# Performance work log

Measured on AMD Instinct MI355X. Metric: run time of the kernel, lower is better.

The kernel has to match this reference:

```python
import jax, jax.numpy as jnp
import numpy as np

B, N, F_NODE = 16, 48, 5
H1, H2 = 32, 64
D_ATT = H2 * 3  # 192


def setup_inputs() -> dict:
    rng = np.random.default_rng(0)
    n_nodes = B * N
    # complete graph per batch element; each directed pair appears with class 0 and class 1,
    # ordered by (src, dst, class) so that filtering src>dst leaves a sorted list where
    # consecutive rows are the (class0, class1) pair of the same undirected edge.
    i, j = np.meshgrid(np.arange(N), np.arange(N), indexing="ij")
    m = i != j
    pi = np.repeat(i[m], 2)
    pj = np.repeat(j[m], 2)
    cls = np.tile(np.array([0.0, 1.0], np.float32), N * (N - 1))
    offs = np.arange(B)[:, None] * N
    src = (pi[None] + offs).ravel()
    dst = (pj[None] + offs).ravel()
    edges = jnp.asarray(np.stack([src, dst]).astype(np.int64))
    w = rng.random(src.shape[0]).astype(np.float32)
    edge_attr = jnp.asarray(np.stack([w, np.tile(cls, B)], axis=1))
    x = jnp.asarray(rng.standard_normal((n_nodes, F_NODE)).astype(np.float32))
    detector_labels = jnp.ones((n_nodes,), bool)
    batch_labels = jnp.asarray(np.repeat(np.arange(B), N).astype(np.int64))

    def lin(k_out, k_in):
        s = 1.0 / np.sqrt(k_in)
        return (jnp.asarray(rng.uniform(-s, s, (k_out, k_in)).astype(np.float32)),
                jnp.asarray(rng.uniform(-s, s, (k_out,)).astype(np.float32)))

    W_we, b_we = lin(1, 3)
    Wrel1, brel1 = lin(H1, F_NODE); Wroot1, _ = lin(H1, F_NODE)
    Wrel2, brel2 = lin(H2, H1);     Wroot2, _ = lin(H2, H1)
    W_ee, b_ee = lin(H2, 3)
    W_qkv, b_qkv = lin(3 * D_ATT, D_ATT)
    W_in, b_in = lin(3 * D_ATT, D_ATT)
    W_out, b_out = lin(D_ATT, D_ATT)
    W_o, b_o = lin(1, D_ATT)
    return dict(x=x, edges=edges, edge_attr=edge_attr,
                detector_labels=detector_labels, batch_labels=batch_labels,
                W_we=W_we, b_we=b_we, Wrel1=Wrel1, brel1=brel1, Wroot1=Wroot1,
                Wrel2=Wrel2, brel2=brel2, Wroot2=Wroot2,
                W_ee=W_ee, b_ee=b_ee, W_qkv=W_qkv, b_qkv=b_qkv,
                W_in=W_in, b_in=b_in, W_out=W_out, b_out=b_out,
                W_o=W_o, b_o=b_o)


def _graph_conv(x, src, dst, w, Wrel, brel, Wroot, n_nodes):
    # pyg GraphConv: lin_rel(sum_{j->i} e_ji * x_j) + lin_root(x_i)
    msg = x[src] * w  # w: [E,1] scalar edge weight
    agg = jax.ops.segment_sum(msg, dst, num_segments=n_nodes)
    return agg @ Wrel.T + brel + x @ Wroot.T


def reference(x, edges, edge_attr, detector_labels, batch_labels,
              W_we, b_we, Wrel1, brel1, Wroot1, Wrel2, brel2, Wroot2,
              W_ee, b_ee, W_qkv, b_qkv, W_in, b_in, W_out, b_out, W_o, b_o):
    n_nodes = x.shape[0]
    E = edges.shape[1]
    src, dst = edges[0], edges[1]
    # edge weight embedding from (weight, one_hot(class))
    c = jax.nn.one_hot(edge_attr[:, 1].astype(jnp.int32), 2, dtype=x.dtype)
    w = jax.nn.relu(jnp.concatenate([edge_attr[:, :1], c], -1) @ W_we.T + b_we)  # [E,1]
    x = jax.nn.relu(_graph_conv(x, src, dst, w, Wrel1, brel1, Wroot1, n_nodes))
    x = jax.nn.relu(_graph_conv(x, src, dst, w, Wrel2, brel2, Wroot2, n_nodes))
    # keep one direction (src > dst): construction guarantees exactly E//2 kept, already sorted
    keep = jnp.nonzero(src > dst, size=E // 2)[0]
    srcK, dstK, ea = src[keep], dst[keep], edge_attr[keep]
    c = jax.nn.one_hot(ea[:, 1].astype(jnp.int32), 2, dtype=x.dtype)
    wK = jax.nn.relu(jnp.concatenate([ea[:, :1], c], -1) @ W_ee.T + b_ee)  # [Ek,H2]
    feat = jnp.concatenate([x[srcK], wK, x[dstK]], -1)  # [Ek, 3*H2]
    # equal-size graphs -> unbatch + pad_sequence == reshape (no padding)
    S = feat.shape[0] // B
    feat = feat.reshape(B, S, -1)
    e_src = srcK.reshape(B, S)
    e_dst = dstK.reshape(B, S)
    classes = ea[:, 1].reshape(B, S, 1)
    pad_mask = e_src == e_dst  # all False (no ragged padding here)
    # SelfAttention: extra qkv projection, then 1-head MultiheadAttention
    qkv = feat @ W_qkv.T + b_qkv
    q, k, v = jnp.split(qkv, 3, -1)
    Wq, Wk, Wv = jnp.split(W_in, 3, 0)
    bq, bk, bv = jnp.split(b_in, 3, 0)
    q = q @ Wq.T + bq; k = k @ Wk.T + bk; v = v @ Wv.T + bv
    scores = jnp.einsum("bqd,bkd->bqk", q, k) / jnp.sqrt(jnp.asarray(q.shape[-1], q.dtype))
    scores = jnp.where(pad_mask[:, None, :], -jnp.inf, scores)
    attn = jax.nn.softmax(scores, -1)
    feat = jnp.einsum("bqk,bkd->bqd", attn, v) @ W_out.T + b_out
    # SplitSyndromes with all-True detector_labels keeps every edge (identity)
    logit = feat @ W_o.T + b_o  # [B,S,1]
    pair = jnp.concatenate([logit[:, ::2], logit[:, 1::2]], -1)   # [B,S/2,2]
    cls2 = jnp.concatenate([classes[:, ::2], classes[:, 1::2]], -1)
    min_inds = jnp.argmin(pair, axis=2, keepdims=True)
    ef = jnp.take_along_axis(pair, min_inds, 2)   # min values, [B,S/2,1]
    ec = jnp.take_along_axis(cls2, min_inds, 2)
    e4s = jnp.stack([e_src[:, ::2], e_src[:, 1::2]], -1)  # [B,S/2,2]
    e4t = jnp.stack([e_dst[:, ::2], e_dst[:, 1::2]], -1)
    out_src = jnp.take_along_axis(e4s, min_inds, -1)
    out_dst = jnp.take_along_axis(e4t, min_inds, -1)
    out_edges = jnp.concatenate([out_src, out_dst], -1)
    return out_edges, ef, ec
```

## Files before the change

### kernel.cpp

```cpp
#include <hip/hip_runtime.h>
#include <hip/hip_bf16.h>

typedef __hip_bfloat16 bf16;
typedef __attribute__((ext_vector_type(8))) short short8;
typedef __attribute__((ext_vector_type(16))) float float16v;
typedef __attribute__((ext_vector_type(2))) float float2v;

#define B_     16
#define N_     48
#define NODES  768
#define PAIRS  2256
#define EK     36096
#define S_     2256
#define SH     1128
#define D_     192
#define KITERS 71
#define QTILES 71
#define QSCALE 0.10411754f

__device__ __forceinline__ float bf(const bf16* p, int i) { return __bfloat162float(p[i]); }
__device__ __forceinline__ float u2f(unsigned short u) {
    return __uint_as_float(((unsigned int)u) << 16);
}
__device__ __forceinline__ float sanitize(float v) {
    if (v > -1e4f && v < 1e4f) return v;
    if (v >= 1e4f) return 1e4f;
    if (v <= -1e4f) return -1e4f;
    return 0.f;
}

__global__ __launch_bounds__(256) void stage1_kernel(
    const bf16* edge_attr, const bf16* W_we, const bf16* b_we, const bf16* x,
    const bf16* Wrel1, const bf16* brel1, const bf16* Wroot1,
    const bf16* Wrel2, const bf16* brel2, const bf16* Wroot2,
    const bf16* W_o, const bf16* b_o, const bf16* W_out, const bf16* b_out,
    const bf16* W_in, const bf16* b_in, const bf16* b_qkv, const bf16* W_qkv,
    float* x2out, float* wo_eff, float* bq_eff, float* bk_eff, float* bv_eff, float* sc,
    float* WqT, float* WkT, bf16* W2b) {
    int blk = blockIdx.x, tid = threadIdx.x;
    if (blk < 16) {
        int b = blk;
        __shared__ float s_ws[N_ * N_];
        __shared__ float s_x[N_ * 5], s_agg1[N_ * 5];
        __shared__ float s_x1[N_ * 32], s_agg2[N_ * 32];
        float we0 = bf(W_we, 0), we1 = bf(W_we, 1), we2 = bf(W_we, 2), bw = bf(b_we, 0);
        for (int idx = tid; idx < N_ * N_; idx += 256) {
            int i = idx / N_, j = idx % N_;
            float v = 0.f;
            if (i != j) {
                int p = i * 47 + (j < i ? j : j - 1);
                int e = (b * PAIRS + p) * 2;
                float w0 = fmaxf(we0 * bf(edge_attr, (e + 0) * 2) + we1 + bw, 0.f);
                float w1 = fmaxf(we0 * bf(edge_attr, (e + 1) * 2) + we2 + bw, 0.f);
                v = w0 + w1;
            }
            s_ws[idx] = v;
        }
        for (int idx = tid; idx < N_ * 5; idx += 256) s_x[idx] = bf(x, b * N_ * 5 + idx);
        __syncthreads();
        if (tid < 240) {
            int j = tid / 5, f = tid % 5;
            float a = 0.f;
            for (int i = 0; i < N_; i++) a += s_ws[i * N_ + j] * s_x[i * 5 + f];
            s_agg1[tid] = a;
        }
        __syncthreads();
        for (int o = tid; o < N_ * 32; o += 256) {
            int j = o >> 5, h = o & 31;
            float a = bf(brel1, h);
            for (int f = 0; f < 5; f++)
                a += bf(Wrel1, h * 5 + f) * s_agg1[j * 5 + f] +
                     bf(Wroot1, h * 5 + f) * s_x[j * 5 + f];
            s_x1[o] = fmaxf(a, 0.f);
        }
        __syncthreads();
        for (int o = tid; o < N_ * 32; o += 256) {
            int j = o >> 5, h = o & 31;
            float a = 0.f;
            for (int i = 0; i < N_; i++) a += s_ws[i * N_ + j] * s_x1[i * 32 + h];
            s_agg2[o] = a;
        }
        __syncthreads();
        for (int o = tid; o < N_ * 64; o += 256) {
            int j = o >> 6, h2 = o & 63;
            float a = bf(brel2, h2);
            for (int h1 = 0; h1 < 32; h1++)
                a += bf(Wrel2, h2 * 32 + h1) * s_agg2[j * 32 + h1] +
                     bf(Wroot2, h2 * 32 + h1) * s_x1[j * 32 + h1];
            x2out[(b * N_ + j) * 64 + h2] = fmaxf(a, 0.f);
        }
    } else if (blk < 209) {
        int a = blk - 16;
        int wave = tid >> 6, lane = tid & 63;
        float partial = 0.f;
        if (a < 192) {
            if (wave == 0) {
                for (int m = lane; m < 192; m += 64)
                    partial += bf(W_o, m) * bf(W_out, m * 192 + a);
            } else {
                int row = (wave - 1) * 192 + a;
                for (int m = lane; m < 192; m += 64)
                    partial += bf(W_in, row * 192 + m) * bf(b_qkv, (wave - 1) * 192 + m);
            }
        } else if (wave == 0) {
            for (int m = lane; m < 192; m += 64) partial += bf(W_o, m) * bf(b_out, m);
        }
        for (int off = 32; off; off >>= 1) partial += __shfl_xor(partial, off, 64);
        if (lane == 0) {
            if (a < 192) {
                if (wave == 0) wo_eff[a] = partial;
                else if (wave == 1) bq_eff[a] = partial + bf(b_in, a);
                else if (wave == 2) bk_eff[a] = partial + bf(b_in, 192 + a);
                else bv_eff[a] = partial + bf(b_in, 384 + a);
            } else if (wave == 0) sc[1] = partial + bf(b_o, 0);
        }
    } else {
        int idx = (blk - 209) * 256 + tid;
        if (idx < D_ * D_) {
            int a = idx / D_, c = idx % D_;
            float acc = 0.f;
            for (int m = 0; m < D_; m++) acc += bf(W_in, a * D_ + m) * bf(W_qkv, m * D_ + c);
            WqT[c * D_ + a] = acc;
            if (c >= 64 && c < 128) W2b[a * 64 + (c - 64)] = __float2bfloat16(acc);
        } else {
            int t = idx - D_ * D_, a = t / D_, c = t % D_;
            float acc = 0.f;
            for (int m = 0; m < D_; m++)
                acc += bf(W_in, (D_ + a) * D_ + m) * bf(W_qkv, (D_ + m) * D_ + c);
            WkT[c * D_ + a] = acc;
            if (c >= 64 && c < 128) W2b[(192 + a) * 64 + (c - 64)] = __float2bfloat16(acc);
        }
    }
}

__global__ __launch_bounds__(256) void stage2_kernel(
    const bf16* W_in, const float* wo_eff, const float* bv_eff,
    const float* x2, const float* WqT, const float* WkT,
    const float* bq_eff, const float* bk_eff,
    float* t_m, float* sc, float* Tq1, float* Tq3, float* Tk1, float* Tk3) {
    int blk = blockIdx.x, tid = threadIdx.x;
    if (blk < 49) {
        int w = blk * 4 + (tid >> 6);
        int lane = tid & 63;
        float partial = 0.f;
        if (w < 192) {
            for (int aa = lane; aa < 192; aa += 64)
                partial += wo_eff[aa] * bf(W_in, (384 + aa) * 192 + w);
        } else if (w == 192) {
            for (int aa = lane; aa < 192; aa += 64) partial += wo_eff[aa] * bv_eff[aa];
        }
        for (int off = 32; off; off >>= 1) partial += __shfl_xor(partial, off, 64);
        if (lane == 0) {
            if (w < 192) t_m[w] = partial;
            else if (w == 192) sc[0] = partial;
        }
    } else {
        int n = blk - 49;
        __shared__ float sx[64];
        if (tid < 64) sx[tid] = x2[n * 64 + tid];
        __syncthreads();
        if (tid < D_) {
            int a = tid;
            float q1 = bq_eff[a], q3 = 0.f, k1 = bk_eff[a], k3 = 0.f;
            for (int c = 0; c < 64; c++) {
                float xv = sx[c];
                q1 += WqT[c * D_ + a] * xv;
                q3 += WqT[(128 + c) * D_ + a] * xv;
                k1 += WkT[c * D_ + a] * xv;
                k3 += WkT[(128 + c) * D_ + a] * xv;
            }
            Tq1[n * D_ + a] = q1; Tq3[n * D_ + a] = q3;
            Tk1[n * D_ + a] = k1; Tk3[n * D_ + a] = k3;
        }
    }
}

__global__ __launch_bounds__(256) void qkvmid_kernel(
    const bf16* edge_attr, const bf16* W_ee, const bf16* b_ee, const bf16* W2b,
    const bf16* W_qkv, const float* t_m, const float* sc, const float* x2,
    const float* Tq1, const float* Tq3, const float* Tk1, const float* Tk3,
    bf16* Q, bf16* K, float* vl) {
    __shared__ short s_w2[384 * 72];
    __shared__ short s_wk[32 * 72];
    __shared__ float s_tm[192], s_wvl[192];
    __shared__ int s_ni[32], s_nj[32];
    __shared__ float s_wraw[32], s_cls[32];
    int tid = threadIdx.x, base = blockIdx.x * 32;

    for (int c = tid; c < 3072; c += 256) {
        int row = c >> 3, off = c & 7;
        uint4 v = *(const uint4*)((const short*)W2b + row * 64 + off * 8);
        *(uint4*)&s_w2[row * 72 + off * 8] = v;
    }
    if (tid < 192) s_tm[tid] = t_m[tid];
    if (tid < 32) {
        int kk_g = base + tid;
        int b = kk_g / S_, kk = kk_g % S_;
        int q = kk >> 1, cls = kk & 1;
        int i = (int)((1.0f + sqrtf(8.0f * (float)q + 1.0f)) * 0.5f);
        while (i * (i - 1) / 2 > q) --i;
        while ((i + 1) * i / 2 <= q) ++i;
        int j = q - i * (i - 1) / 2;
        s_ni[tid] = b * N_ + i; s_nj[tid] = b * N_ + j;
        int e = (b * PAIRS + i * 47 + j) * 2 + cls;
        s_wraw[tid] = bf(edge_attr, e * 2);
        s_cls[tid] = (float)cls;
    }
    __syncthreads();
    for (int idx = tid; idx < 32 * 64; idx += 256) {
        int t = idx >> 6, h = idx & 63;
        int cls = (int)s_cls[t];
        float v = bf(W_ee, h * 3) * s_wraw[t] + bf(W_ee, h * 3 + 1 + cls) + bf(b_ee, h);
        bf16 bv = __float2bfloat16(fmaxf(v, 0.f));
        s_wk[t * 72 + h] = *reinterpret_cast<short*>(&bv);
    }
    if (tid < 192) {
        float acc = 0.f;
        for (int m = 0; m < 192; m++) acc += s_tm[m] * bf(W_qkv, (384 + m) * 192 + tid);
        s_wvl[tid] = acc;
    }
    __syncthreads();

    int wave = tid >> 6, lane = tid & 63;
    int l5 = lane & 31, h5 = lane >> 5;

    short8 af[4];
    #pragma unroll
    for (int kc = 0; kc < 4; kc++)
        af[kc] = *(const short8*)&s_wk[l5 * 72 + kc * 16 + h5 * 8];

    int tl[16], niv[16], njv[16];
    #pragma unroll
    for (int r = 0; r < 16; r++) {
        int t = (r & 3) + 8 * (r >> 2) + 4 * h5;
        tl[r] = t; niv[r] = s_ni[t]; njv[r] = s_nj[t];
    }

    #pragma unroll
    for (int tt = 0; tt < 3; tt++) {
        int ta = wave + tt * 4;
        bool isq = ta < 6;
        int ag = (isq ? ta : ta - 6) * 32 + l5;
        float16v c;
        #pragma unroll
        for (int r = 0; r < 16; r++) c[r] = 0.f;
        #pragma unroll
        for (int kc = 0; kc < 4; kc++) {
            short8 bfr = *(const short8*)&s_w2[(ta * 32 + l5) * 72 + kc * 16 + h5 * 8];
            c = __builtin_amdgcn_mfma_f32_32x32x16_bf16(af[kc], bfr, c, 0, 0, 0);
        }
        const float* T1 = isq ? Tq1 : Tk1;
        const float* T3 = isq ? Tq3 : Tk3;
        bf16* Out = isq ? Q : K;
        #pragma unroll
        for (int r = 0; r < 16; r++) {
            float v = c[r] + T1[niv[r] * D_ + ag] + T3[njv[r] * D_ + ag];
            if (isq) v *= QSCALE;
            Out[(long)(base + tl[r]) * D_ + ag] = __float2bfloat16(v);
        }
    }
    if (tid < 32) {
        float v = sc[0];
        const float* xi = &x2[s_ni[tid] * 64];
        const float* xj = &x2[s_nj[tid] * 64];
        for (int h = 0; h < 64; h++) {
            v += s_wvl[h] * xi[h] + s_wvl[128 + h] * xj[h] +
                 s_wvl[64 + h] * u2f((unsigned short)s_wk[tid * 72 + h]);
        }
        vl[base + tid] = v;
    }
}

__global__ __launch_bounds__(512) void attn_kernel(const bf16* Q, const bf16* K,
                                                   const float* vl, float* part) {
    int x = blockIdx.x;
    int rr = x & 7, rest = x >> 3;
    int hi = rest >= 72;
    int b = rr + 8 * hi;
    int s = rest - 72 * hi;
    int chunk = s / 9, qg = s % 9;
    int tid = threadIdx.x;
    int wave = tid >> 6, lane = tid & 63;
    int n5 = lane & 31, h5 = lane >> 5;
    int qt = qg * 8 + wave;
    bool qvalid = qt < QTILES;
    int t0 = chunk * 9;
    int nit = (chunk == 7) ? 8 : 9;

    __shared__ short s_k[2][32 * 200];
    __shared__ float s_vl[2][32];

    int row0 = tid / 24, cc0 = tid % 24;
    int c1 = tid + 512;
    int row1 = c1 / 24, cc1 = c1 % 24;
    bool has1 = tid < 256;

    short8 qf[12];
    {
        int qrow = b * S_ + qt * 32 + n5;
        if (qrow > B_ * S_ - 1) qrow = B_ * S_ - 1;
        const short* qp = (const short*)Q + (long)qrow * D_;
        #pragma unroll
        for (int kc = 0; kc < 12; kc++) qf[kc] = *(const short8*)(qp + kc * 16 + h5 * 8);
    }

    float lr[16], ar[16];
    #pragma unroll
    for (int r = 0; r < 16; r++) { lr[r] = 0.f; ar[r] = 0.f; }

    uint4 p0, p1; float pv = 0.f;
    {
        int key = t0 * 32 + row0;
        int gk = b * S_ + (key < S_ ? key : S_ - 1);
        p0 = *(const uint4*)((const short*)K + (long)gk * D_ + cc0 * 8);
        if (has1) {
            int key1 = t0 * 32 + row1;
            int gk1 = b * S_ + (key1 < S_ ? key1 : S_ - 1);
            p1 = *(const uint4*)((const short*)K + (long)gk1 * D_ + cc1 * 8);
        }
        if (tid < 32) {
            int key2 = t0 * 32 + tid;
            pv = (key2 < S_) ? vl[b * S_ + key2] : 0.f;
        }
    }

    for (int k = 0; k < nit; ++k) {
        int it = t0 + k;
        int buf = k & 1;
        *(uint4*)&s_k[buf][row0 * 200 + cc0 * 8] = p0;
        if (has1) *(uint4*)&s_k[buf][row1 * 200 + cc1 * 8] = p1;
        if (tid < 32) s_vl[buf][tid] = pv;
        if (k + 1 < nit) {
            int it1 = it + 1;
            int key = it1 * 32 + row0;
            int gk = b * S_ + (key < S_ ? key : S_ - 1);
            p0 = *(const uint4*)((const short*)K + (long)gk * D_ + cc0 * 8);
            if (has1) {
                int key1 = it1 * 32 + row1;
                int gk1 = b * S_ + (key1 < S_ ? key1 : S_ - 1);
                p1 = *(const uint4*)((const short*)K + (long)gk1 * D_ + cc1 * 8);
            }
            if (tid < 32) {
                int key2 = it1 * 32 + tid;
                pv = (key2 < S_) ? vl[b * S_ + key2] : 0.f;
            }
        }
        __syncthreads();
        const short* kb = s_k[buf];
        float16v c;
        #pragma unroll
        for (int r = 0; r < 16; r++) c[r] = 0.f;
        #pragma unroll
        for (int kc = 0; kc < 12; kc++) {
            short8 bfr = *(const short8*)(kb + n5 * 200 + kc * 16 + h5 * 8);
            c = __builtin_amdgcn_mfma_f32_32x32x16_bf16(qf[kc], bfr, c, 0, 0, 0);
        }
        float vlv = s_vl[buf][n5];
        if (it != KITERS - 1) {
            #pragma unroll
            for (int r = 0; r < 16; r++) {
                float p = __builtin_amdgcn_exp2f(c[r]);
                lr[r] += p;
                ar[r] += p * vlv;
            }
        } else {
            bool kv = n5 < 16;
            #pragma unroll
            for (int r = 0; r < 16; r++) {
                float p = kv ? __builtin_amdgcn_exp2f(c[r]) : 0.f;
                lr[r] += p;
                ar[r] += p * vlv;
            }
        }
    }

    if (qvalid) {
        #pragma unroll
        for (int r = 0; r < 16; r++) {
            float l = lr[r], a = ar[r];
            #pragma unroll
            for (int off = 1; off < 32; off <<= 1) {
                l += __shfl_xor(l, off, 64);
                a += __shfl_xor(a, off, 64);
            }
            if (n5 == 0) {
                int qrow = qt * 32 + (r & 3) + 8 * (r >> 2) + 4 * h5;
                if (qrow < S_) {
                    float2v pv2 = {l, a};
                    *(float2v*)&part[((long)(b * S_ + qrow) * 8 + chunk) * 2] = pv2;
                }
            }
        }
    }
}

__global__ __launch_bounds__(256) void final_kernel(const float* part, const float* sc,
                                                    float* out) {
    int idx = blockIdx.x * 256 + threadIdx.x;
    if (idx >= B_ * SH) return;
    int b = idx / SH, p = idx % SH;
    int i = (int)((1.0f + sqrtf(8.0f * (float)p + 1.0f)) * 0.5f);
    while (i * (i - 1) / 2 > p) --i;
    while ((i + 1) * i / 2 <= p) ++i;
    int j = p - i * (i - 1) / 2;
    float co = sc[1];
    float lg[2];
    #pragma unroll
    for (int t = 0; t < 2; t++) {
        long g = (long)b * S_ + 2 * p + t;
        float l = 0.f, a = 0.f;
        #pragma unroll
        for (int c = 0; c < 8; c++) {
            float2v pc = *(const float2v*)&part[(g * 8 + c) * 2];
            l += pc.x;
            a += pc.y;
        }
        lg[t] = sanitize(a / l + co);
    }
    int ind = (lg[1] < lg[0]) ? 1 : 0;
    float ef = ind ? lg[1] : lg[0];
    out[(b * SH + p) * 2 + 0] = (float)(b * N_ + i);
    out[(b * SH + p) * 2 + 1] = (float)(b * N_ + j);
    out[2 * B_ * SH + idx] = ef;
    out[2 * B_ * SH + B_ * SH + idx] = (float)ind;
}

extern "C" void kernel_launch(void* const* d_in, const int* in_sizes, int n_in,
                              void* d_out, int out_size, void* d_ws, size_t ws_size,
                              hipStream_t stream) {
    const bf16* x         = (const bf16*)d_in[0];
    const bf16* edge_attr = (const bf16*)d_in[2];
    const bf16* W_we   = (const bf16*)d_in[5];
    const bf16* b_we   = (const bf16*)d_in[6];
    const bf16* Wrel1  = (const bf16*)d_in[7];
    const bf16* brel1  = (const bf16*)d_in[8];
    const bf16* Wroot1 = (const bf16*)d_in[9];
    const bf16* Wrel2  = (const bf16*)d_in[10];
    const bf16* brel2  = (const bf16*)d_in[11];
    const bf16* Wroot2 = (const bf16*)d_in[12];
    const bf16* W_ee   = (const bf16*)d_in[13];
    const bf16* b_ee   = (const bf16*)d_in[14];
    const bf16* W_qkv  = (const bf16*)d_in[15];
    const bf16* b_qkv  = (const bf16*)d_in[16];
    const bf16* W_in   = (const bf16*)d_in[17];
    const bf16* b_in   = (const bf16*)d_in[18];
    const bf16* W_out  = (const bf16*)d_in[19];
    const bf16* b_out  = (const bf16*)d_in[20];
    const bf16* W_o    = (const bf16*)d_in[21];
    const bf16* b_o    = (const bf16*)d_in[22];

    float* w = (float*)d_ws;
    float* WqT    = w;
    float* WkT    = WqT + 36864;
    float* t_m    = WkT + 36864;
    float* bq_eff = t_m + 192;
    float* bk_eff = bq_eff + 192;
    float* bv_eff = bk_eff + 192;
    float* wo_eff = bv_eff + 192;
    float* sc     = wo_eff + 192;
    float* x2     = sc + 64;
    float* vl     = x2 + 49152;
    float* part   = vl + 36096;
    bf16*  Q      = (bf16*)(part + 577536);
    bf16*  K      = Q + (long)EK * D_;
    bf16*  W2b    = K + (long)EK * D_;
    float* Tq1    = (float*)(W2b + 384 * 64);
    float* Tq3    = Tq1 + NODES * D_;
    float* Tk1    = Tq3 + NODES * D_;
    float* Tk3    = Tk1 + NODES * D_;

    stage1_kernel<<<497, 256, 0, stream>>>(edge_attr, W_we, b_we, x, Wrel1, brel1, Wroot1,
                                           Wrel2, brel2, Wroot2, W_o, b_o, W_out, b_out,
                                           W_in, b_in, b_qkv, W_qkv,
                                           x2, wo_eff, bq_eff, bk_eff, bv_eff, sc,
                                           WqT, WkT, W2b);
    stage2_kernel<<<817, 256, 0, stream>>>(W_in, wo_eff, bv_eff, x2, WqT, WkT,
                                           bq_eff, bk_eff, t_m, sc, Tq1, Tq3, Tk1, Tk3);
    qkvmid_kernel<<<EK / 32, 256, 0, stream>>>(edge_attr, W_ee, b_ee, W2b, W_qkv, t_m, sc, x2,
                                               Tq1, Tq3, Tk1, Tk3, Q, K, vl);
    attn_kernel<<<1152, 512, 0, stream>>>(Q, K, vl, part);
    final_kernel<<<(B_ * SH + 255) / 256, 256, 0, stream>>>(part, sc, (float*)d_out);
}
```

Before: 256.8 us.

## Compute two query tiles per wave in attention and hoist wvl projection

The attention kernel now uses 256-thread blocks where each wave computes two 32-row query tiles against the same K fragment from shared memory, so each K read from LDS feeds twice as many MFMAs. K staging is redistributed over three loads per thread. Separately, the per-block 192x192 wvl reduction that every qkvmid block recomputed is moved into a small dedicated kernel. The vl dot products are also spread over all 256 threads with shuffle reductions. The cost is higher register pressure from doubled Q fragments and accumulators, plus one extra kernel launch.

```diff
diff --git a/kernel.cpp b/kernel.cpp
--- a/kernel.cpp
+++ b/kernel.cpp
@@ -175,14 +175,26 @@
     }
 }
 
+__global__ __launch_bounds__(256) void wvl_kernel(const bf16* W_qkv, const float* t_m,
+                                                  float* wvl) {
+    int w = blockIdx.x * 4 + (threadIdx.x >> 6);
+    int lane = threadIdx.x & 63;
+    if (w >= 192) return;
+    float partial = 0.f;
+    for (int m = lane; m < 192; m += 64)
+        partial += t_m[m] * bf(W_qkv, (384 + m) * 192 + w);
+    for (int off = 32; off; off >>= 1) partial += __shfl_xor(partial, off, 64);
+    if (lane == 0) wvl[w] = partial;
+}
+
 __global__ __launch_bounds__(256) void qkvmid_kernel(
     const bf16* edge_attr, const bf16* W_ee, const bf16* b_ee, const bf16* W2b,
-    const bf16* W_qkv, const float* t_m, const float* sc, const float* x2,
+    const float* wvl, const float* sc, const float* x2,
     const float* Tq1, const float* Tq3, const float* Tk1, const float* Tk3,
     bf16* Q, bf16* K, float* vl) {
     __shared__ short s_w2[384 * 72];
     __shared__ short s_wk[32 * 72];
-    __shared__ float s_tm[192], s_wvl[192];
+    __shared__ float s_wvl[192];
     __shared__ int s_ni[32], s_nj[32];
     __shared__ float s_wraw[32], s_cls[32];
     int tid = threadIdx.x, base = blockIdx.x * 32;
@@ -192,7 +204,7 @@
         uint4 v = *(const uint4*)((const short*)W2b + row * 64 + off * 8);
         *(uint4*)&s_w2[row * 72 + off * 8] = v;
     }
-    if (tid < 192) s_tm[tid] = t_m[tid];
+    if (tid < 192) s_wvl[tid] = wvl[tid];
     if (tid < 32) {
         int kk_g = base + tid;
         int b = kk_g / S_, kk = kk_g % S_;
@@ -214,11 +226,6 @@
         bf16 bv = __float2bfloat16(fmaxf(v, 0.f));
         s_wk[t * 72 + h] = *reinterpret_cast<short*>(&bv);
     }
-    if (tid < 192) {
-        float acc = 0.f;
-        for (int m = 0; m < 192; m++) acc += s_tm[m] * bf(W_qkv, (384 + m) * 192 + tid);
-        s_wvl[tid] = acc;
-    }
     __syncthreads();
 
     int wave = tid >> 6, lane = tid & 63;
@@ -259,20 +266,26 @@
             Out[(long)(base + tl[r]) * D_ + ag] = __float2bfloat16(v);
         }
     }
-    if (tid < 32) {
-        float v = sc[0];
-        const float* xi = &x2[s_ni[tid] * 64];
-        const float* xj = &x2[s_nj[tid] * 64];
-        for (int h = 0; h < 64; h++) {
+    {
+        int t = tid >> 3, g = tid & 7;
+        const float* xi = &x2[s_ni[t] * 64];
+        const float* xj = &x2[s_nj[t] * 64];
+        float v = 0.f;
+        #pragma unroll
+        for (int hh = 0; hh < 8; hh++) {
+            int h = g * 8 + hh;
             v += s_wvl[h] * xi[h] + s_wvl[128 + h] * xj[h] +
-                 s_wvl[64 + h] * u2f((unsigned short)s_wk[tid * 72 + h]);
-        }
-        vl[base + tid] = v;
-    }
-}
-
-__global__ __launch_bounds__(512) void attn_kernel(const bf16* Q, const bf16* K,
-                                                   const float* vl, float* part) {
+                 s_wvl[64 + h] * u2f((unsigned short)s_wk[t * 72 + h]);
+        }
+        v += __shfl_xor(v, 1, 64);
+        v += __shfl_xor(v, 2, 64);
+        v += __shfl_xor(v, 4, 64);
+        if (g == 0) vl[base + t] = v + sc[0];
+    }
+}
+
+__global__ __launch_bounds__(256, 2) void attn_kernel(const bf16* Q, const bf16* K,
+                                                      const float* vl, float* part) {
     int x = blockIdx.x;
     int rr = x & 7, rest = x >> 3;
     int hi = rest >= 72;
@@ -282,109 +295,124 @@
     int tid = threadIdx.x;
     int wave = tid >> 6, lane = tid & 63;
     int n5 = lane & 31, h5 = lane >> 5;
-    int qt = qg * 8 + wave;
-    bool qvalid = qt < QTILES;
+    int qtA = qg * 8 + wave * 2;
+    int qtB = qtA + 1;
+    bool validB = qtB < QTILES;
     int t0 = chunk * 9;
     int nit = (chunk == 7) ? 8 : 9;
 
     __shared__ short s_k[2][32 * 200];
     __shared__ float s_vl[2][32];
 
-    int row0 = tid / 24, cc0 = tid % 24;
-    int c1 = tid + 512;
-    int row1 = c1 / 24, cc1 = c1 % 24;
-    bool has1 = tid < 256;
-
-    short8 qf[12];
+    int r0 = tid / 24, c0 = tid % 24;
+    int r1 = (tid + 256) / 24, c1 = (tid + 256) % 24;
+    int r2 = (tid + 512) / 24, c2 = (tid + 512) % 24;
+
+    short8 qfA[12], qfB[12];
     {
-        int qrow = b * S_ + qt * 32 + n5;
-        if (qrow > B_ * S_ - 1) qrow = B_ * S_ - 1;
-        const short* qp = (const short*)Q + (long)qrow * D_;
-        #pragma unroll
-        for (int kc = 0; kc < 12; kc++) qf[kc] = *(const short8*)(qp + kc * 16 + h5 * 8);
-    }
-
-    float lr[16], ar[16];
+        int qrowA = b * S_ + qtA * 32 + n5;
+        int qrowB = b * S_ + qtB * 32 + n5;
+        if (qrowB > B_ * S_ - 1) qrowB = B_ * S_ - 1;
+        const short* qpA = (const short*)Q + (long)qrowA * D_;
+        const short* qpB = (const short*)Q + (long)qrowB * D_;
+        #pragma unroll
+        for (int kc = 0; kc < 12; kc++) {
+            qfA[kc] = *(const short8*)(qpA + kc * 16 + h5 * 8);
+            qfB[kc] = *(const short8*)(qpB + kc * 16 + h5 * 8);
+        }
+    }
+
+    float lrA[16], arA[16], lrB[16], arB[16];
     #pragma unroll
-    for (int r = 0; r < 16; r++) { lr[r] = 0.f; ar[r] = 0.f; }
-
-    uint4 p0, p1; float pv = 0.f;
+    for (int r = 0; r < 16; r++) { lrA[r] = 0.f; arA[r] = 0.f; lrB[r] = 0.f; arB[r] = 0.f; }
+
+    uint4 p0, p1, p2; float pv = 0.f;
     {
-        int key = t0 * 32 + row0;
-        int gk = b * S_ + (key < S_ ? key : S_ - 1);
-        p0 = *(const uint4*)((const short*)K + (long)gk * D_ + cc0 * 8);
-        if (has1) {
-            int key1 = t0 * 32 + row1;
-            int gk1 = b * S_ + (key1 < S_ ? key1 : S_ - 1);
-            p1 = *(const uint4*)((const short*)K + (long)gk1 * D_ + cc1 * 8);
-        }
+        int k0 = t0 * 32 + r0, k1 = t0 * 32 + r1, k2 = t0 * 32 + r2;
+        p0 = *(const uint4*)((const short*)K + (long)(b * S_ + (k0 < S_ ? k0 : S_ - 1)) * D_ + c0 * 8);
+        p1 = *(const uint4*)((const short*)K + (long)(b * S_ + (k1 < S_ ? k1 : S_ - 1)) * D_ + c1 * 8);
+        p2 = *(const uint4*)((const short*)K + (long)(b * S_ + (k2 < S_ ? k2 : S_ - 1)) * D_ + c2 * 8);
         if (tid < 32) {
-            int key2 = t0 * 32 + tid;
-            pv = (key2 < S_) ? vl[b * S_ + key2] : 0.f;
+            int key = t0 * 32 + tid;
+            pv = (key < S_) ? vl[b * S_ + key] : 0.f;
         }
     }
 
     for (int k = 0; k < nit; ++k) {
         int it = t0 + k;
         int buf = k & 1;
-        *(uint4*)&s_k[buf][row0 * 200 + cc0 * 8] = p0;
-        if (has1) *(uint4*)&s_k[buf][row1 * 200 + cc1 * 8] = p1;
+        *(uint4*)&s_k[buf][r0 * 200 + c0 * 8] = p0;
+        *(uint4*)&s_k[buf][r1 * 200 + c1 * 8] = p1;
+        *(uint4*)&s_k[buf][r2 * 200 + c2 * 8] = p2;
         if (tid < 32) s_vl[buf][tid] = pv;
         if (k + 1 < nit) {
             int it1 = it + 1;
-            int key = it1 * 32 + row0;
-            int gk = b * S_ + (key < S_ ? key : S_ - 1);
-            p0 = *(const uint4*)((const short*)K + (long)gk * D_ + cc0 * 8);
-            if (has1) {
-                int key1 = it1 * 32 + row1;
-                int gk1 = b * S_ + (key1 < S_ ? key1 : S_ - 1);
-                p1 = *(const uint4*)((const short*)K + (long)gk1 * D_ + cc1 * 8);
-            }
+            int k0 = it1 * 32 + r0, k1 = it1 * 32 + r1, k2 = it1 * 32 + r2;
+            p0 = *(const uint4*)((const short*)K + (long)(b * S_ + (k0 < S_ ? k0 : S_ - 1)) * D_ + c0 * 8);
+            p1 = *(const uint4*)((const short*)K + (long)(b * S_ + (k1 < S_ ? k1 : S_ - 1)) * D_ + c1 * 8);
+            p2 = *(const uint4*)((const short*)K + (long)(b * S_ + (k2 < S_ ? k2 : S_ - 1)) * D_ + c2 * 8);
             if (tid < 32) {
-                int key2 = it1 * 32 + tid;
-                pv = (key2 < S_) ? vl[b * S_ + key2] : 0.f;
+                int key = it1 * 32 + tid;
+                pv = (key < S_) ? vl[b * S_ + key] : 0.f;
             }
         }
         __syncthreads();
         const short* kb = s_k[buf];
-        float16v c;
-        #pragma unroll
-        for (int r = 0; r < 16; r++) c[r] = 0.f;
+        float16v cA, cB;
+        #pragma unroll
+        for (int r = 0; r < 16; r++) { cA[r] = 0.f; cB[r] = 0.f; }
         #pragma unroll
         for (int kc = 0; kc < 12; kc++) {
             short8 bfr = *(const short8*)(kb + n5 * 200 + kc * 16 + h5 * 8);
-            c = __builtin_amdgcn_mfma_f32_32x32x16_bf16(qf[kc], bfr, c, 0, 0, 0);
+            cA = __builtin_amdgcn_mfma_f32_32x32x16_bf16(qfA[kc], bfr, cA, 0, 0, 0);
+            cB = __builtin_amdgcn_mfma_f32_32x32x16_bf16(qfB[kc], bfr, cB, 0, 0, 0);
         }
         float vlv = s_vl[buf][n5];
         if (it != KITERS - 1) {
             #pragma unroll
             for (int r = 0; r < 16; r++) {
-                float p = __builtin_amdgcn_exp2f(c[r]);
-                lr[r] += p;
-                ar[r] += p * vlv;
+                float pA = __builtin_amdgcn_exp2f(cA[r]);
+                float pB = __builtin_amdgcn_exp2f(cB[r]);
+                lrA[r] += pA; arA[r] += pA * vlv;
+                lrB[r] += pB; arB[r] += pB * vlv;
             }
         } else {
             bool kv = n5 < 16;
             #pragma unroll
             for (int r = 0; r < 16; r++) {
-                float p = kv ? __builtin_amdgcn_exp2f(c[r]) : 0.f;
-                lr[r] += p;
-                ar[r] += p * vlv;
-            }
-        }
-    }
-
-    if (qvalid) {
+                float pA = kv ? __builtin_amdgcn_exp2f(cA[r]) : 0.f;
+                float pB = kv ? __builtin_amdgcn_exp2f(cB[r]) : 0.f;
+                lrA[r] += pA; arA[r] += pA * vlv;
+                lrB[r] += pB; arB[r] += pB * vlv;
+            }
+        }
+    }
+
+    #pragma unroll
+    for (int r = 0; r < 16; r++) {
+        float l = lrA[r], a = arA[r];
+        #pragma unroll
+        for (int off = 1; off < 32; off <<= 1) {
+            l += __shfl_xor(l, off, 64);
+            a += __shfl_xor(a, off, 64);
+        }
+        if (n5 == 0) {
+            int qrow = qtA * 32 + (r & 3) + 8 * (r >> 2) + 4 * h5;
+            float2v pv2 = {l, a};
+            *(float2v*)&part[((long)(b * S_ + qrow) * 8 + chunk) * 2] = pv2;
+        }
+    }
+    if (validB) {
         #pragma unroll
         for (int r = 0; r < 16; r++) {
-            float l = lr[r], a = ar[r];
+            float l = lrB[r], a = arB[r];
             #pragma unroll
             for (int off = 1; off < 32; off <<= 1) {
                 l += __shfl_xor(l, off, 64);
                 a += __shfl_xor(a, off, 64);
             }
             if (n5 == 0) {
-                int qrow = qt * 32 + (r & 3) + 8 * (r >> 2) + 4 * h5;
+                int qrow = qtB * 32 + (r & 3) + 8 * (r >> 2) + 4 * h5;
                 if (qrow < S_) {
                     float2v pv2 = {l, a};
                     *(float2v*)&part[((long)(b * S_ + qrow) * 8 + chunk) * 2] = pv2;
@@ -457,7 +485,8 @@
     float* bk_eff = bq_eff + 192;
     float* bv_eff = bk_eff + 192;
     float* wo_eff = bv_eff + 192;
-    float* sc     = wo_eff + 192;
+    float* wvl    = wo_eff + 192;
+    float* sc     = wvl + 192;
     float* x2     = sc + 64;
     float* vl     = x2 + 49152;
     float* part   = vl + 36096;
@@ -476,8 +505,9 @@
                                            WqT, WkT, W2b);
     stage2_kernel<<<817, 256, 0, stream>>>(W_in, wo_eff, bv_eff, x2, WqT, WkT,
                                            bq_eff, bk_eff, t_m, sc, Tq1, Tq3, Tk1, Tk3);
-    qkvmid_kernel<<<EK / 32, 256, 0, stream>>>(edge_attr, W_ee, b_ee, W2b, W_qkv, t_m, sc, x2,
+    wvl_kernel<<<48, 256, 0, stream>>>(W_qkv, t_m, wvl);
+    qkvmid_kernel<<<EK / 32, 256, 0, stream>>>(edge_attr, W_ee, b_ee, W2b, wvl, sc, x2,
                                                Tq1, Tq3, Tk1, Tk3, Q, K, vl);
-    attn_kernel<<<1152, 512, 0, stream>>>(Q, K, vl, part);
+    attn_kernel<<<1152, 256, 0, stream>>>(Q, K, vl, part);
     final_kernel<<<(B_ * SH + 255) / 256, 256, 0, stream>>>(part, sc, (float*)d_out);
 }
```

New measurement: 300.1 us. 1.17x slower.

## Hoist wvl reduction into separate kernel and load W2b fragments into registers

Applied to the files above, without the earlier changes.

The 192x192 wvl dot product that every qkvmid block recomputed is moved into a small dedicated kernel run once, and qkvmid now just reads the result. The W2b weight tile is loaded straight from global memory into MFMA B-operand registers instead of being staged through a 55KB shared-memory buffer. This frees LDS for higher occupancy and removes a sync-bound copy. The vl dot product is also spread across all 256 threads with a shuffle reduction instead of 32 serial threads. Costs are an extra kernel launch and more registers per thread.

```diff
diff --git a/kernel.cpp b/kernel.cpp
--- a/kernel.cpp
+++ b/kernel.cpp
@@ -175,24 +175,42 @@
     }
 }
 
+__global__ __launch_bounds__(256) void wvl_kernel(const bf16* W_qkv, const float* t_m,
+                                                  float* wvl) {
+    int w = blockIdx.x * 4 + (threadIdx.x >> 6);
+    int lane = threadIdx.x & 63;
+    if (w >= 192) return;
+    float partial = 0.f;
+    for (int m = lane; m < 192; m += 64)
+        partial += t_m[m] * bf(W_qkv, (384 + m) * 192 + w);
+    for (int off = 32; off; off >>= 1) partial += __shfl_xor(partial, off, 64);
+    if (lane == 0) wvl[w] = partial;
+}
+
 __global__ __launch_bounds__(256) void qkvmid_kernel(
     const bf16* edge_attr, const bf16* W_ee, const bf16* b_ee, const bf16* W2b,
-    const bf16* W_qkv, const float* t_m, const float* sc, const float* x2,
+    const float* wvl, const float* sc, const float* x2,
     const float* Tq1, const float* Tq3, const float* Tk1, const float* Tk3,
     bf16* Q, bf16* K, float* vl) {
-    __shared__ short s_w2[384 * 72];
     __shared__ short s_wk[32 * 72];
-    __shared__ float s_tm[192], s_wvl[192];
+    __shared__ float s_wvl[192];
     __shared__ int s_ni[32], s_nj[32];
     __shared__ float s_wraw[32], s_cls[32];
     int tid = threadIdx.x, base = blockIdx.x * 32;
-
-    for (int c = tid; c < 3072; c += 256) {
-        int row = c >> 3, off = c & 7;
-        uint4 v = *(const uint4*)((const short*)W2b + row * 64 + off * 8);
-        *(uint4*)&s_w2[row * 72 + off * 8] = v;
-    }
-    if (tid < 192) s_tm[tid] = t_m[tid];
+    int wave = tid >> 6, lane = tid & 63;
+    int l5 = lane & 31, h5 = lane >> 5;
+
+    short8 bfr[3][4];
+    #pragma unroll
+    for (int tt = 0; tt < 3; tt++) {
+        int ta = wave + tt * 4;
+        const short* wrow = (const short*)W2b + (ta * 32 + l5) * 64;
+        #pragma unroll
+        for (int kc = 0; kc < 4; kc++)
+            bfr[tt][kc] = *(const short8*)(wrow + kc * 16 + h5 * 8);
+    }
+
+    if (tid < 192) s_wvl[tid] = wvl[tid];
     if (tid < 32) {
         int kk_g = base + tid;
         int b = kk_g / S_, kk = kk_g % S_;
@@ -214,15 +232,7 @@
         bf16 bv = __float2bfloat16(fmaxf(v, 0.f));
         s_wk[t * 72 + h] = *reinterpret_cast<short*>(&bv);
     }
-    if (tid < 192) {
-        float acc = 0.f;
-        for (int m = 0; m < 192; m++) acc += s_tm[m] * bf(W_qkv, (384 + m) * 192 + tid);
-        s_wvl[tid] = acc;
-    }
     __syncthreads();
-
-    int wave = tid >> 6, lane = tid & 63;
-    int l5 = lane & 31, h5 = lane >> 5;
 
     short8 af[4];
     #pragma unroll
@@ -245,10 +255,8 @@
         #pragma unroll
         for (int r = 0; r < 16; r++) c[r] = 0.f;
         #pragma unroll
-        for (int kc = 0; kc < 4; kc++) {
-            short8 bfr = *(const short8*)&s_w2[(ta * 32 + l5) * 72 + kc * 16 + h5 * 8];
-            c = __builtin_amdgcn_mfma_f32_32x32x16_bf16(af[kc], bfr, c, 0, 0, 0);
-        }
+        for (int kc = 0; kc < 4; kc++)
+            c = __builtin_amdgcn_mfma_f32_32x32x16_bf16(af[kc], bfr[tt][kc], c, 0, 0, 0);
         const float* T1 = isq ? Tq1 : Tk1;
         const float* T3 = isq ? Tq3 : Tk3;
         bf16* Out = isq ? Q : K;
@@ -259,15 +267,21 @@
             Out[(long)(base + tl[r]) * D_ + ag] = __float2bfloat16(v);
         }
     }
-    if (tid < 32) {
-        float v = sc[0];
-        const float* xi = &x2[s_ni[tid] * 64];
-        const float* xj = &x2[s_nj[tid] * 64];
-        for (int h = 0; h < 64; h++) {
+    {
+        int t = tid >> 3, g = tid & 7;
+        const float* xi = &x2[s_ni[t] * 64];
+        const float* xj = &x2[s_nj[t] * 64];
+        float v = 0.f;
+        #pragma unroll
+        for (int hh = 0; hh < 8; hh++) {
+            int h = g * 8 + hh;
             v += s_wvl[h] * xi[h] + s_wvl[128 + h] * xj[h] +
-                 s_wvl[64 + h] * u2f((unsigned short)s_wk[tid * 72 + h]);
-        }
-        vl[base + tid] = v;
+                 s_wvl[64 + h] * u2f((unsigned short)s_wk[t * 72 + h]);
+        }
+        v += __shfl_xor(v, 1, 64);
+        v += __shfl_xor(v, 2, 64);
+        v += __shfl_xor(v, 4, 64);
+        if (g == 0) vl[base + t] = v + sc[0];
     }
 }
 
@@ -457,7 +471,8 @@
     float* bk_eff = bq_eff + 192;
     float* bv_eff = bk_eff + 192;
     float* wo_eff = bv_eff + 192;
-    float* sc     = wo_eff + 192;
+    float* wvl    = wo_eff + 192;
+    float* sc     = wvl + 192;
     float* x2     = sc + 64;
     float* vl     = x2 + 49152;
     float* part   = vl + 36096;
@@ -476,7 +491,8 @@
                                            WqT, WkT, W2b);
     stage2_kernel<<<817, 256, 0, stream>>>(W_in, wo_eff, bv_eff, x2, WqT, WkT,
                                            bq_eff, bk_eff, t_m, sc, Tq1, Tq3, Tk1, Tk3);
-    qkvmid_kernel<<<EK / 32, 256, 0, stream>>>(edge_attr, W_ee, b_ee, W2b, W_qkv, t_m, sc, x2,
+    wvl_kernel<<<48, 256, 0, stream>>>(W_qkv, t_m, wvl);
+    qkvmid_kernel<<<EK / 32, 256, 0, stream>>>(edge_attr, W_ee, b_ee, W2b, wvl, sc, x2,
                                                Tq1, Tq3, Tk1, Tk3, Q, K, vl);
     attn_kernel<<<1152, 512, 0, stream>>>(Q, K, vl, part);
     final_kernel<<<(B_ * SH + 255) / 256, 256, 0, stream>>>(part, sc, (float*)d_out);
```

New measurement: 239.8 us. 6.6% less time.
